# Kernel tuning notes

Hardware: AMD Instinct MI355X
Metric: run time of the kernel (lower is better)

The kernel has to match this reference:

```python
import jax, jax.numpy as jnp
import numpy as np

NEG = -1000000000.0

def setup_inputs() -> dict:
    key = jax.random.key(0)
    ks = jax.random.split(key, 6)
    B, V, F, H = 8, 4, 256, 768
    video_features = jax.random.normal(ks[0], (B, V, F, H), dtype=jnp.float32)
    video_attention_mask = jax.random.randint(ks[1], (B, V, F), 0, 2) > 0  # True = masked
    s = 1.0 / np.sqrt(H)
    Wqkv = jax.random.normal(ks[2], (3 * H, H), dtype=jnp.float32) * s
    bqkv = jax.random.normal(ks[3], (3 * H,), dtype=jnp.float32) * 0.01
    Wo = jax.random.normal(ks[4], (H, H), dtype=jnp.float32) * s
    bo = jax.random.normal(ks[5], (H,), dtype=jnp.float32) * 0.01
    return {"video_features": video_features, "video_attention_mask": video_attention_mask,
            "Wqkv": Wqkv, "bqkv": bqkv, "Wo": Wo, "bo": bo}

def reference(video_features, video_attention_mask, Wqkv, bqkv, Wo, bo):
    B, V, F, H = video_features.shape
    n_heads = 12
    head_dim = H // n_heads
    S = V * F  # total frames
    x = video_features.reshape(B, S, H)
    mask = video_attention_mask.reshape(B, S)
    # fused QKV projection (torch Linear: x @ W.T + b)
    qkv = x @ Wqkv.T + bqkv                      # [B, S, 3H]
    qkv = qkv.reshape(B, S, n_heads, 3 * head_dim).transpose(0, 2, 1, 3)  # [B, h, S, 3d]
    q, k, v = jnp.split(qkv, 3, axis=-1)         # each [B, h, S, d]
    scores = jnp.einsum('bhqd,bhkd->bhqk', q, k) / np.sqrt(head_dim)
    scores = jnp.where(mask[:, None, None, :], NEG, scores)
    attn = jax.nn.softmax(scores, axis=-1)       # dropout p=0 (eval) -> identity
    out = jnp.einsum('bhqk,bhkd->bhqd', attn, v) # [B, h, S, d]
    out = out.transpose(0, 2, 1, 3).reshape(B, S, H)
    out = out @ Wo.T + bo
    return out.reshape(B, V, F, H)
```

## Files before the change

kernel.cpp:

```cpp
#include <hip/hip_runtime.h>
#include <stdint.h>

typedef unsigned short u16;
typedef unsigned int u32;
typedef __attribute__((ext_vector_type(8))) unsigned short u16x8;
typedef __attribute__((ext_vector_type(4))) unsigned short u16x4;
typedef __attribute__((ext_vector_type(4))) float f32x4;
typedef __attribute__((ext_vector_type(16))) float f32x16;
typedef __attribute__((ext_vector_type(4))) float floatx4;
typedef __attribute__((ext_vector_type(8))) __bf16 bf16x8;


__device__ __forceinline__ u16 f2bf(float f) {
  union { float f; unsigned u; } c; c.f = f;
  unsigned r = c.u + 0x7fffu + ((c.u >> 16) & 1u);
  return (u16)(r >> 16);
}

__device__ __forceinline__ u32 packbf2(float lo, float hi) {
  return (u32)f2bf(lo) | ((u32)f2bf(hi) << 16);
}

__device__ __forceinline__ bf16x8 ld_bf8(const u16* p) {
  return __builtin_bit_cast(bf16x8, *(const u16x8*)p);
}

__device__ __forceinline__ float fexp2(float x) {
#if __has_builtin(__builtin_amdgcn_exp2f)
  return __builtin_amdgcn_exp2f(x);
#else
  float r; asm("v_exp_f32 %0, %1" : "=v"(r) : "v"(x)); return r;
#endif
}

__device__ __forceinline__ void glds16(const void* g, void* l) {
  __builtin_amdgcn_global_load_lds(
      (const __attribute__((address_space(1))) void*)g,
      (__attribute__((address_space(3))) void*)l, 16, 0, 0);
}

__global__ void convert_kernel(const float* __restrict__ x,
                               const float* __restrict__ w1,
                               const float* __restrict__ w2,
                               u16* __restrict__ xb,
                               u16* __restrict__ w1b,
                               u16* __restrict__ w2b) {
  const long NX = 6291456 / 4, NW1 = 1769472 / 4, NW2 = 589824 / 4;
  const long total = NX + NW1 + NW2;
  for (long i = (long)blockIdx.x * 256 + threadIdx.x; i < total;
       i += (long)gridDim.x * 256) {
    const float* src; u16* dst; long j;
    if (i < NX)            { src = x;  dst = xb;  j = i; }
    else if (i < NX + NW1) { src = w1; dst = w1b; j = i - NX; }
    else                   { src = w2; dst = w2b; j = i - NX - NW1; }
    floatx4 v = ((const floatx4*)src)[j];
    u16x4 o;
    o[0] = f2bf(v[0]); o[1] = f2bf(v[1]); o[2] = f2bf(v[2]); o[3] = f2bf(v[3]);
    ((u16x4*)dst)[j] = o;
  }
}

__global__ __launch_bounds__(256, 3)
void qkv_gemm(const u16* __restrict__ A, const u16* __restrict__ W,
              const float* __restrict__ bias,
              u16* __restrict__ qb, u16* __restrict__ kb, u16* __restrict__ vtb) {
  __shared__ __align__(16) u16 lA[128 * 64];
  __shared__ __align__(16) u16 lB[128 * 64];
  const int tid = threadIdx.x;
  const int lane = tid & 63, wid = tid >> 6;
  const int wm = wid >> 1, wn = wid & 1;
  const int l15 = lane & 15, l4 = lane >> 4;
  const int h7 = l15 & 7;
  const int rowA0 = blockIdx.y * 128, rowB0 = blockIdx.x * 128;

  const int rlo = lane >> 3;
  const int swz = (lane & 7) ^ rlo;
  const u16* ga = A + (size_t)(rowA0 + wid * 8 + rlo) * 768 + swz * 8;
  const u16* gb = W + (size_t)(rowB0 + wid * 8 + rlo) * 768 + swz * 8;

  f32x4 acc[4][4];
  const f32x4 vz = {0.f, 0.f, 0.f, 0.f};
#pragma unroll
  for (int i = 0; i < 4; ++i)
#pragma unroll
    for (int j = 0; j < 4; ++j) acc[i][j] = vz;

  for (int k0 = 0; k0 < 768; k0 += 64) {
#pragma unroll
    for (int j = 0; j < 4; ++j) {
      glds16(ga + k0 + j * 32 * 768, lA + j * 2048 + wid * 512);
      glds16(gb + k0 + j * 32 * 768, lB + j * 2048 + wid * 512);
    }
    __syncthreads();
    bf16x8 af[4][2], bfr[4][2];
#pragma unroll
    for (int mi = 0; mi < 4; ++mi)
#pragma unroll
      for (int ks = 0; ks < 2; ++ks)
        af[mi][ks] = ld_bf8(lA + (wm * 64 + mi * 16 + l15) * 64 +
                            (((ks * 4 + l4) ^ h7) * 8));
#pragma unroll
    for (int ni = 0; ni < 4; ++ni)
#pragma unroll
      for (int ks = 0; ks < 2; ++ks)
        bfr[ni][ks] = ld_bf8(lB + (wn * 64 + ni * 16 + l15) * 64 +
                             (((ks * 4 + l4) ^ h7) * 8));
#pragma unroll
    for (int mi = 0; mi < 4; ++mi)
#pragma unroll
      for (int ni = 0; ni < 4; ++ni)
#pragma unroll
        for (int ks = 0; ks < 2; ++ks)
          acc[mi][ni] = __builtin_amdgcn_mfma_f32_16x16x32_bf16(
              af[mi][ks], bfr[ni][ks], acc[mi][ni], 0, 0, 0);
    __syncthreads();
  }

  const float QSC = 0.125f * 1.44269504088896f;
#pragma unroll
  for (int ni = 0; ni < 4; ++ni) {
    int n = rowB0 + wn * 64 + ni * 16 + l15;
    int h = n / 192;
    int r3 = n - h * 192;
    int t = r3 >> 6, dd = r3 & 63;
    float bn_ = bias[n];
#pragma unroll
    for (int mi = 0; mi < 4; ++mi) {
#pragma unroll
      for (int r = 0; r < 4; ++r) {
        int m = rowA0 + wm * 64 + mi * 16 + l4 * 4 + r;
        int b = m >> 10, s = m & 1023;
        size_t bh = (size_t)(b * 12 + h);
        float v = acc[mi][ni][r] + bn_;
        if (t == 0)
          qb[bh * 65536 + (size_t)s * 64 + dd] = f2bf(v * QSC);
        else if (t == 1)
          kb[bh * 65536 + (size_t)s * 64 + dd] = f2bf(v);
        else
          vtb[bh * 65536 + (size_t)dd * 1024 + s] = f2bf(v);
      }
    }
  }
}

__global__ __launch_bounds__(256, 3)
void attn_kernel(const u16* __restrict__ qb, const u16* __restrict__ kb,
                 const u16* __restrict__ vtb, const void* __restrict__ maskp,
                 u16* __restrict__ x2) {
  const int bh = blockIdx.x, qt = blockIdx.y;
  const int b = bh / 12, h = bh - b * 12;
  const int tid = threadIdx.x;
  const int w = tid >> 6, lane = tid & 63;
  const int l31 = lane & 31, hi = lane >> 5;

  __shared__ float mbias[1024];
  __shared__ int any_big;
  __shared__ __align__(16) u16 plds[4][32][40];
  __shared__ __align__(16) u16 kvs[16384];

  if (tid == 0) any_big = 0;
  __syncthreads();
  {
    const unsigned* mu = (const unsigned*)maskp;
    int loc = 0;
    for (int i = tid; i < 2048; i += 256)
      if (mu[i] > 1u) loc = 1;
    if (loc) atomicOr(&any_big, 1);
  }
  __syncthreads();
  const float CEXP = 23.0831206542234f;
  if (any_big) {
    const unsigned char* mb = (const unsigned char*)maskp;
    for (int i = tid; i < 1024; i += 256)
      mbias[i] = mb[b * 1024 + i] ? -100000.0f : -CEXP;
  } else {
    const int* mi_ = (const int*)maskp;
    for (int i = tid; i < 1024; i += 256)
      mbias[i] = mi_[b * 1024 + i] ? -100000.0f : -CEXP;
  }

  const size_t base = (size_t)bh * 65536;
  const int q0w = qt * 128 + w * 32;

  const int rlo = lane >> 3;
  const int cg = (lane & 7) ^ (rlo & 7);
  const int srow = w * 8 + rlo;
  const u16* kg0 = kb + base + (size_t)srow * 64 + cg * 8;
  const u16* vg0 = vtb + base + (size_t)srow * 1024 + cg * 8;
  u16* kd0 = kvs + w * 512;
  u16* vd0 = kvs + 4096 + w * 512;

  bf16x8 qf[4];
#pragma unroll
  for (int dstep = 0; dstep < 4; ++dstep)
    qf[dstep] = ld_bf8(qb + base + (size_t)(q0w + l31) * 64 + dstep * 16 + hi * 8);

  f32x16 o[2];
#pragma unroll
  for (int dh = 0; dh < 2; ++dh)
#pragma unroll
    for (int r = 0; r < 16; ++r) o[dh][r] = 0.f;
  float ps = 0.f;

  glds16(kg0, kd0);
  glds16(kg0 + 32 * 64, kd0 + 2048);
  glds16(vg0, vd0);
  glds16(vg0 + 32 * 1024, vd0 + 2048);
  __syncthreads();

  for (int kt = 0; kt < 16; ++kt) {
    const int cur = kt & 1;
    if (kt < 15) {
      const int nxt = cur ^ 1;
      glds16(kg0 + (kt + 1) * 4096, kd0 + nxt * 8192);
      glds16(kg0 + (kt + 1) * 4096 + 32 * 64, kd0 + nxt * 8192 + 2048);
      glds16(vg0 + (kt + 1) * 64, vd0 + nxt * 8192);
      glds16(vg0 + (kt + 1) * 64 + 32 * 1024, vd0 + nxt * 8192 + 2048);
    }

    const u16* Kl = kvs + cur * 8192;
    const u16* Vl = kvs + cur * 8192 + 4096;

#pragma unroll
    for (int kk = 0; kk < 2; ++kk) {
      f32x16 s;
#pragma unroll
      for (int r = 0; r < 16; ++r) s[r] = 0.f;
      const int rk = kk * 32 + l31;
      __builtin_amdgcn_s_setprio(1);
#pragma unroll
      for (int dstep = 0; dstep < 4; ++dstep) {
        bf16x8 kf = ld_bf8(Kl + rk * 64 + ((dstep * 2 + hi) ^ (rk & 7)) * 8);
        s = __builtin_amdgcn_mfma_f32_32x32x16_bf16(kf, qf[dstep], s, 0, 0, 0);
      }
      __builtin_amdgcn_s_setprio(0);
#pragma unroll
      for (int g = 0; g < 4; ++g) {
        f32x4 bv = *(const f32x4*)(mbias + kt * 64 + kk * 32 + g * 8 + hi * 4);
        float p0 = fexp2(s[g * 4 + 0] + bv[0]);
        float p1 = fexp2(s[g * 4 + 1] + bv[1]);
        float p2 = fexp2(s[g * 4 + 2] + bv[2]);
        float p3 = fexp2(s[g * 4 + 3] + bv[3]);
        ps += (p0 + p1) + (p2 + p3);
        const int colb = g * 8 + hi * 4;
        *(u32*)&plds[w][l31][colb]     = packbf2(p0, p1);
        *(u32*)&plds[w][l31][colb + 2] = packbf2(p2, p3);
      }

      __builtin_amdgcn_s_setprio(1);
#pragma unroll
      for (int t = 0; t < 2; ++t) {
        bf16x8 pf = ld_bf8(&plds[w][l31][t * 16 + hi * 8]);
#pragma unroll
        for (int dh = 0; dh < 2; ++dh) {
          const int rv = dh * 32 + l31;
          const int gv = kk * 4 + t * 2 + hi;
          bf16x8 vf = ld_bf8(Vl + rv * 64 + (gv ^ (rv & 7)) * 8);
          o[dh] = __builtin_amdgcn_mfma_f32_32x32x16_bf16(vf, pf, o[dh], 0, 0, 0);
        }
      }
      __builtin_amdgcn_s_setprio(0);
    }

    __syncthreads();
  }

  ps += __shfl_xor(ps, 32, 64);
  float inv = 1.0f / ps;

  u16* obuf = kvs + w * 2304;
#pragma unroll
  for (int dh = 0; dh < 2; ++dh)
#pragma unroll
    for (int j = 0; j < 8; ++j) {
      u32 v = packbf2(o[dh][2 * j] * inv, o[dh][2 * j + 1] * inv);
      int col = dh * 32 + 8 * (j >> 1) + 4 * hi + 2 * (j & 1);
      *(u32*)(obuf + l31 * 72 + col) = v;
    }

  {
    int row2 = lane >> 1, ch = lane & 1;
    const u16* srcp = obuf + row2 * 72 + ch * 32;
    u16x8 t0 = *(const u16x8*)(srcp);
    u16x8 t1 = *(const u16x8*)(srcp + 8);
    u16x8 t2 = *(const u16x8*)(srcp + 16);
    u16x8 t3 = *(const u16x8*)(srcp + 24);
    size_t m = (size_t)b * 1024 + qt * 128 + w * 32 + row2;
    u16* dst = x2 + m * 768 + h * 64 + ch * 32;
    *(u16x8*)dst = t0;
    *(u16x8*)(dst + 8) = t1;
    *(u16x8*)(dst + 16) = t2;
    *(u16x8*)(dst + 24) = t3;
  }
}

__global__ __launch_bounds__(256, 3)
void out_gemm(const u16* __restrict__ A, const u16* __restrict__ W,
              const float* __restrict__ bias, float* __restrict__ out) {
  __shared__ __align__(16) u16 lA[128 * 64];
  __shared__ __align__(16) u16 lB[128 * 64];
  const int tid = threadIdx.x;
  const int lane = tid & 63, wid = tid >> 6;
  const int wm = wid >> 1, wn = wid & 1;
  const int l15 = lane & 15, l4 = lane >> 4;
  const int h7 = l15 & 7;
  const int rowA0 = blockIdx.y * 128, rowB0 = blockIdx.x * 128;

  const int rlo = lane >> 3;
  const int swz = (lane & 7) ^ rlo;
  const u16* ga = A + (size_t)(rowA0 + wid * 8 + rlo) * 768 + swz * 8;
  const u16* gb = W + (size_t)(rowB0 + wid * 8 + rlo) * 768 + swz * 8;

  f32x4 acc[4][4];
  const f32x4 vz = {0.f, 0.f, 0.f, 0.f};
#pragma unroll
  for (int i = 0; i < 4; ++i)
#pragma unroll
    for (int j = 0; j < 4; ++j) acc[i][j] = vz;

  for (int k0 = 0; k0 < 768; k0 += 64) {
#pragma unroll
    for (int j = 0; j < 4; ++j) {
      glds16(ga + k0 + j * 32 * 768, lA + j * 2048 + wid * 512);
      glds16(gb + k0 + j * 32 * 768, lB + j * 2048 + wid * 512);
    }
    __syncthreads();
    bf16x8 af[4][2], bfr[4][2];
#pragma unroll
    for (int mi = 0; mi < 4; ++mi)
#pragma unroll
      for (int ks = 0; ks < 2; ++ks)
        af[mi][ks] = ld_bf8(lA + (wm * 64 + mi * 16 + l15) * 64 +
                            (((ks * 4 + l4) ^ h7) * 8));
#pragma unroll
    for (int ni = 0; ni < 4; ++ni)
#pragma unroll
      for (int ks = 0; ks < 2; ++ks)
        bfr[ni][ks] = ld_bf8(lB + (wn * 64 + ni * 16 + l15) * 64 +
                             (((ks * 4 + l4) ^ h7) * 8));
#pragma unroll
    for (int mi = 0; mi < 4; ++mi)
#pragma unroll
      for (int ni = 0; ni < 4; ++ni)
#pragma unroll
        for (int ks = 0; ks < 2; ++ks)
          acc[mi][ni] = __builtin_amdgcn_mfma_f32_16x16x32_bf16(
              af[mi][ks], bfr[ni][ks], acc[mi][ni], 0, 0, 0);
    __syncthreads();
  }

#pragma unroll
  for (int ni = 0; ni < 4; ++ni) {
    int n = rowB0 + wn * 64 + ni * 16 + l15;
    float bn_ = bias[n];
#pragma unroll
    for (int mi = 0; mi < 4; ++mi)
#pragma unroll
      for (int r = 0; r < 4; ++r) {
        int m = rowA0 + wm * 64 + mi * 16 + l4 * 4 + r;
        out[(size_t)m * 768 + n] = acc[mi][ni][r] + bn_;
      }
  }
}

extern "C" void kernel_launch(void* const* d_in, const int* in_sizes, int n_in,
                              void* d_out, int out_size, void* d_ws, size_t ws_size,
                              hipStream_t stream) {
  const float* x    = (const float*)d_in[0];
  const void*  mask = d_in[1];
  const float* wqkv = (const float*)d_in[2];
  const float* bqkv = (const float*)d_in[3];
  const float* wo   = (const float*)d_in[4];
  const float* bo   = (const float*)d_in[5];
  float* out = (float*)d_out;

  u16* ws = (u16*)d_ws;
  u16* xbf   = ws;
  u16* wqkvb = ws + 6291456;
  u16* wob   = ws + 8060928;
  u16* qbuf  = ws + 8650752;
  u16* kbuf  = ws + 14942208;
  u16* vtbuf = ws + 21233664;
  u16* x2buf = ws + 27525120;

  convert_kernel<<<2048, 256, 0, stream>>>(x, wqkv, wo, xbf, wqkvb, wob);
  qkv_gemm<<<dim3(18, 64), 256, 0, stream>>>(xbf, wqkvb, bqkv, qbuf, kbuf, vtbuf);
  attn_kernel<<<dim3(96, 8), 256, 0, stream>>>(qbuf, kbuf, vtbuf, mask, x2buf);
  out_gemm<<<dim3(6, 64), 256, 0, stream>>>(x2buf, wob, bo, out);
}
```

Before: 133.2 us.

## Double-buffer LDS in QKV and output GEMMs with XCD-aware block remap

Both GEMM kernels now use two LDS buffers so the next K-tile's global-to-LDS loads are issued before computing on the current tile, which halves the barriers per iteration and overlaps memory with MFMA. Grids become 1D, with block ids remapped so consecutive blocks on the same XCD share A-row tiles for better L2 reuse. MFMA sections are bracketed with s_setprio. LDS doubles to 64KB per block and launch bounds drop to 2 blocks per CU, which reduces occupancy.

```diff
diff --git a/kernel.cpp b/kernel.cpp
--- a/kernel.cpp
+++ b/kernel.cpp
@@ -60,18 +60,23 @@
   }
 }
 
-__global__ __launch_bounds__(256, 3)
+__global__ __launch_bounds__(256, 2)
 void qkv_gemm(const u16* __restrict__ A, const u16* __restrict__ W,
               const float* __restrict__ bias,
               u16* __restrict__ qb, u16* __restrict__ kb, u16* __restrict__ vtb) {
-  __shared__ __align__(16) u16 lA[128 * 64];
-  __shared__ __align__(16) u16 lB[128 * 64];
+  __shared__ __align__(16) u16 lA[2][128 * 64];
+  __shared__ __align__(16) u16 lB[2][128 * 64];
   const int tid = threadIdx.x;
   const int lane = tid & 63, wid = tid >> 6;
   const int wm = wid >> 1, wn = wid & 1;
   const int l15 = lane & 15, l4 = lane >> 4;
   const int h7 = l15 & 7;
-  const int rowA0 = blockIdx.y * 128, rowB0 = blockIdx.x * 128;
+
+  const int p = blockIdx.x;
+  const int xcd = p & 7, i = p >> 3;
+  const int by = xcd * 8 + i / 18;
+  const int bx = i % 18;
+  const int rowA0 = by * 128, rowB0 = bx * 128;
 
   const int rlo = lane >> 3;
   const int swz = (lane & 7) ^ rlo;
@@ -81,40 +86,51 @@
   f32x4 acc[4][4];
   const f32x4 vz = {0.f, 0.f, 0.f, 0.f};
 #pragma unroll
-  for (int i = 0; i < 4; ++i)
-#pragma unroll
-    for (int j = 0; j < 4; ++j) acc[i][j] = vz;
-
-  for (int k0 = 0; k0 < 768; k0 += 64) {
-#pragma unroll
-    for (int j = 0; j < 4; ++j) {
-      glds16(ga + k0 + j * 32 * 768, lA + j * 2048 + wid * 512);
-      glds16(gb + k0 + j * 32 * 768, lB + j * 2048 + wid * 512);
-    }
+  for (int ii = 0; ii < 4; ++ii)
+#pragma unroll
+    for (int j = 0; j < 4; ++j) acc[ii][j] = vz;
+
+#define QSTAGE(buf, k0)                                          \
+  {                                                              \
+    _Pragma("unroll") for (int j = 0; j < 4; ++j) {              \
+      glds16(ga + (k0) + j * 32 * 768, lA[buf] + j * 2048 + wid * 512); \
+      glds16(gb + (k0) + j * 32 * 768, lB[buf] + j * 2048 + wid * 512); \
+    }                                                            \
+  }
+
+  QSTAGE(0, 0);
+  __syncthreads();
+
+  for (int ks = 0; ks < 12; ++ks) {
+    const int cur = ks & 1;
+    if (ks < 11) QSTAGE(cur ^ 1, (ks + 1) * 64);
+
+    bf16x8 af[4][2], bfr[4][2];
+#pragma unroll
+    for (int mi = 0; mi < 4; ++mi)
+#pragma unroll
+      for (int kk = 0; kk < 2; ++kk)
+        af[mi][kk] = ld_bf8(lA[cur] + (wm * 64 + mi * 16 + l15) * 64 +
+                            (((kk * 4 + l4) ^ h7) * 8));
+#pragma unroll
+    for (int ni = 0; ni < 4; ++ni)
+#pragma unroll
+      for (int kk = 0; kk < 2; ++kk)
+        bfr[ni][kk] = ld_bf8(lB[cur] + (wn * 64 + ni * 16 + l15) * 64 +
+                             (((kk * 4 + l4) ^ h7) * 8));
+    __builtin_amdgcn_s_setprio(1);
+#pragma unroll
+    for (int mi = 0; mi < 4; ++mi)
+#pragma unroll
+      for (int ni = 0; ni < 4; ++ni)
+#pragma unroll
+        for (int kk = 0; kk < 2; ++kk)
+          acc[mi][ni] = __builtin_amdgcn_mfma_f32_16x16x32_bf16(
+              af[mi][kk], bfr[ni][kk], acc[mi][ni], 0, 0, 0);
+    __builtin_amdgcn_s_setprio(0);
     __syncthreads();
-    bf16x8 af[4][2], bfr[4][2];
-#pragma unroll
-    for (int mi = 0; mi < 4; ++mi)
-#pragma unroll
-      for (int ks = 0; ks < 2; ++ks)
-        af[mi][ks] = ld_bf8(lA + (wm * 64 + mi * 16 + l15) * 64 +
-                            (((ks * 4 + l4) ^ h7) * 8));
-#pragma unroll
-    for (int ni = 0; ni < 4; ++ni)
-#pragma unroll
-      for (int ks = 0; ks < 2; ++ks)
-        bfr[ni][ks] = ld_bf8(lB + (wn * 64 + ni * 16 + l15) * 64 +
-                             (((ks * 4 + l4) ^ h7) * 8));
-#pragma unroll
-    for (int mi = 0; mi < 4; ++mi)
-#pragma unroll
-      for (int ni = 0; ni < 4; ++ni)
-#pragma unroll
-        for (int ks = 0; ks < 2; ++ks)
-          acc[mi][ni] = __builtin_amdgcn_mfma_f32_16x16x32_bf16(
-              af[mi][ks], bfr[ni][ks], acc[mi][ni], 0, 0, 0);
-    __syncthreads();
-  }
+  }
+#undef QSTAGE
 
   const float QSC = 0.125f * 1.44269504088896f;
 #pragma unroll
@@ -294,17 +310,22 @@
   }
 }
 
-__global__ __launch_bounds__(256, 3)
+__global__ __launch_bounds__(256, 2)
 void out_gemm(const u16* __restrict__ A, const u16* __restrict__ W,
               const float* __restrict__ bias, float* __restrict__ out) {
-  __shared__ __align__(16) u16 lA[128 * 64];
-  __shared__ __align__(16) u16 lB[128 * 64];
+  __shared__ __align__(16) u16 lA[2][128 * 64];
+  __shared__ __align__(16) u16 lB[2][128 * 64];
   const int tid = threadIdx.x;
   const int lane = tid & 63, wid = tid >> 6;
   const int wm = wid >> 1, wn = wid & 1;
   const int l15 = lane & 15, l4 = lane >> 4;
   const int h7 = l15 & 7;
-  const int rowA0 = blockIdx.y * 128, rowB0 = blockIdx.x * 128;
+
+  const int p = blockIdx.x;
+  const int xcd = p & 7, i = p >> 3;
+  const int by = xcd * 8 + i / 6;
+  const int bx = i % 6;
+  const int rowA0 = by * 128, rowB0 = bx * 128;
 
   const int rlo = lane >> 3;
   const int swz = (lane & 7) ^ rlo;
@@ -314,40 +335,51 @@
   f32x4 acc[4][4];
   const f32x4 vz = {0.f, 0.f, 0.f, 0.f};
 #pragma unroll
-  for (int i = 0; i < 4; ++i)
-#pragma unroll
-    for (int j = 0; j < 4; ++j) acc[i][j] = vz;
-
-  for (int k0 = 0; k0 < 768; k0 += 64) {
-#pragma unroll
-    for (int j = 0; j < 4; ++j) {
-      glds16(ga + k0 + j * 32 * 768, lA + j * 2048 + wid * 512);
-      glds16(gb + k0 + j * 32 * 768, lB + j * 2048 + wid * 512);
-    }
+  for (int ii = 0; ii < 4; ++ii)
+#pragma unroll
+    for (int j = 0; j < 4; ++j) acc[ii][j] = vz;
+
+#define OSTAGE(buf, k0)                                          \
+  {                                                              \
+    _Pragma("unroll") for (int j = 0; j < 4; ++j) {              \
+      glds16(ga + (k0) + j * 32 * 768, lA[buf] + j * 2048 + wid * 512); \
+      glds16(gb + (k0) + j * 32 * 768, lB[buf] + j * 2048 + wid * 512); \
+    }                                                            \
+  }
+
+  OSTAGE(0, 0);
+  __syncthreads();
+
+  for (int ks = 0; ks < 12; ++ks) {
+    const int cur = ks & 1;
+    if (ks < 11) OSTAGE(cur ^ 1, (ks + 1) * 64);
+
+    bf16x8 af[4][2], bfr[4][2];
+#pragma unroll
+    for (int mi = 0; mi < 4; ++mi)
+#pragma unroll
+      for (int kk = 0; kk < 2; ++kk)
+        af[mi][kk] = ld_bf8(lA[cur] + (wm * 64 + mi * 16 + l15) * 64 +
+                            (((kk * 4 + l4) ^ h7) * 8));
+#pragma unroll
+    for (int ni = 0; ni < 4; ++ni)
+#pragma unroll
+      for (int kk = 0; kk < 2; ++kk)
+        bfr[ni][kk] = ld_bf8(lB[cur] + (wn * 64 + ni * 16 + l15) * 64 +
+                             (((kk * 4 + l4) ^ h7) * 8));
+    __builtin_amdgcn_s_setprio(1);
+#pragma unroll
+    for (int mi = 0; mi < 4; ++mi)
+#pragma unroll
+      for (int ni = 0; ni < 4; ++ni)
+#pragma unroll
+        for (int kk = 0; kk < 2; ++kk)
+          acc[mi][ni] = __builtin_amdgcn_mfma_f32_16x16x32_bf16(
+              af[mi][kk], bfr[ni][kk], acc[mi][ni], 0, 0, 0);
+    __builtin_amdgcn_s_setprio(0);
     __syncthreads();
-    bf16x8 af[4][2], bfr[4][2];
-#pragma unroll
-    for (int mi = 0; mi < 4; ++mi)
-#pragma unroll
-      for (int ks = 0; ks < 2; ++ks)
-        af[mi][ks] = ld_bf8(lA + (wm * 64 + mi * 16 + l15) * 64 +
-                            (((ks * 4 + l4) ^ h7) * 8));
-#pragma unroll
-    for (int ni = 0; ni < 4; ++ni)
-#pragma unroll
-      for (int ks = 0; ks < 2; ++ks)
-        bfr[ni][ks] = ld_bf8(lB + (wn * 64 + ni * 16 + l15) * 64 +
-                             (((ks * 4 + l4) ^ h7) * 8));
-#pragma unroll
-    for (int mi = 0; mi < 4; ++mi)
-#pragma unroll
-      for (int ni = 0; ni < 4; ++ni)
-#pragma unroll
-        for (int ks = 0; ks < 2; ++ks)
-          acc[mi][ni] = __builtin_amdgcn_mfma_f32_16x16x32_bf16(
-              af[mi][ks], bfr[ni][ks], acc[mi][ni], 0, 0, 0);
-    __syncthreads();
-  }
+  }
+#undef OSTAGE
 
 #pragma unroll
   for (int ni = 0; ni < 4; ++ni) {
@@ -384,7 +416,7 @@
   u16* x2buf = ws + 27525120;
 
   convert_kernel<<<2048, 256, 0, stream>>>(x, wqkv, wo, xbf, wqkvb, wob);
-  qkv_gemm<<<dim3(18, 64), 256, 0, stream>>>(xbf, wqkvb, bqkv, qbuf, kbuf, vtbuf);
+  qkv_gemm<<<1152, 256, 0, stream>>>(xbf, wqkvb, bqkv, qbuf, kbuf, vtbuf);
   attn_kernel<<<dim3(96, 8), 256, 0, stream>>>(qbuf, kbuf, vtbuf, mask, x2buf);
-  out_gemm<<<dim3(6, 64), 256, 0, stream>>>(x2buf, wob, bo, out);
-}
+  out_gemm<<<384, 256, 0, stream>>>(x2buf, wob, bo, out);
+}
```

New measurement: 131.1 us. No clear change (-1.6%).
